# Optimization experiments

Hardware: AMD Instinct MI355X
Metric: run time of the kernel (lower is better)

## Reference

```python
import jax, jax.numpy as jnp
import numpy as np

N_NODES = 50000
N_EDGES = 800000
IN_F, HID_F, OUT_F = 128, 64, 32
N_GRAPHS = 128


def setup_inputs() -> dict:
    key = jax.random.key(0)
    ks = jax.random.split(key, 8)
    x = jax.random.normal(ks[0], (N_NODES, IN_F), dtype=jnp.float32)
    edge_index = jax.random.randint(ks[1], (2, N_EDGES), 0, N_NODES, dtype=jnp.int64)
    edge_features = jax.random.uniform(ks[2], (N_EDGES,), dtype=jnp.float32)
    batch = jnp.sort(jax.random.randint(ks[3], (N_NODES,), 0, N_GRAPHS, dtype=jnp.int64))
    W = jax.random.normal(ks[4], (IN_F, HID_F), dtype=jnp.float32) / np.sqrt(IN_F)
    b = jax.random.normal(ks[5], (HID_F,), dtype=jnp.float32) * 0.01
    W1 = jax.random.normal(ks[6], (HID_F, OUT_F), dtype=jnp.float32) / np.sqrt(HID_F)
    b1 = jax.random.normal(ks[7], (OUT_F,), dtype=jnp.float32) * 0.01
    return {"x": x, "edge_index": edge_index, "edge_features": edge_features,
            "batch": batch, "num_graphs": N_GRAPHS, "W": W, "b": b, "W1": W1, "b1": b1}


def _gcn_conv(x, edge_index, edge_weight, W, b):
    # Standard GCNConv: add self-loops (weight 1), symmetric normalization,
    # transform-then-aggregate.
    n = x.shape[0]
    loop = jnp.arange(n, dtype=edge_index.dtype)
    src = jnp.concatenate([edge_index[0], loop])
    dst = jnp.concatenate([edge_index[1], loop])
    ew = jnp.concatenate([edge_weight, jnp.ones((n,), edge_weight.dtype)])
    deg = jax.ops.segment_sum(ew, dst, num_segments=n)          # [N]
    dinv = jnp.where(deg > 0, jax.lax.rsqrt(deg), 0.0)
    norm = dinv[src] * ew * dinv[dst]                           # [E+N]
    h = x @ W                                                   # [N, H]
    msg = h[src] * norm[:, None]                                # gather + scale
    out = jax.ops.segment_sum(msg, dst, num_segments=n)         # scatter-add
    return out + b


def reference(x, edge_index, edge_features, batch, num_graphs, W, b, W1, b1):
    h = _gcn_conv(x, edge_index, edge_features, W, b)
    h = jnp.tanh(h)
    # dropout is identity at inference
    node_embeddings = h
    sums = jax.ops.segment_sum(h, batch, num_segments=num_graphs)           # [G, H]
    cnts = jax.ops.segment_sum(jnp.ones((h.shape[0],), h.dtype), batch,
                               num_segments=num_graphs)                      # [G]
    graph_embeddings = sums / jnp.maximum(cnts, 1.0)[:, None]
    graph_embeddings = jnp.tanh(graph_embeddings @ W1 + b1)
    return (graph_embeddings, node_embeddings)
```

## Files before the change

### kernel.cpp

```cpp
#include <hip/hip_runtime.h>
#include <hip/hip_fp16.h>
#include <math.h>

#define N_NODES  50000
#define N_EDGES  800000
#define IN_F     128
#define HID_F    64
#define OUT_F    32
#define N_GRAPHS 128
#define SCAN_BLOCKS  ((N_NODES + 255) / 256)
#define GEMM_BLOCKS  ((N_NODES + 127) / 128)
#define HISTO_BLOCKS ((N_EDGES + 255) / 256)

__global__ __launch_bounds__(256) void fused_gemm_histo(const float* __restrict__ x,
                                                        const float* __restrict__ W,
                                                        __half* __restrict__ hs_h,
                                                        const int* __restrict__ dst,
                                                        int* __restrict__ cnt,
                                                        int* __restrict__ epos) {
    __shared__ float Ws[IN_F][HID_F];
    if (blockIdx.x >= GEMM_BLOCKS) {
        int e = (blockIdx.x - GEMM_BLOCKS) * 256 + threadIdx.x;
        if (e < N_EDGES) epos[e] = atomicAdd(&cnt[dst[e]], 1);
        return;
    }

    int tid = threadIdx.x;
    for (int i = tid * 4; i < IN_F * HID_F; i += 256 * 4) {
        *(float4*)&((float*)Ws)[i] = *(const float4*)&W[i];
    }
    __syncthreads();

    int r0 = blockIdx.x * 128 + (tid >> 2);
    int r1 = r0 + 64;
    int c0 = (tid & 3) * 16;
    if (r0 >= N_NODES) return;
    bool has1 = (r1 < N_NODES);

    float acc0[16], acc1[16];
#pragma unroll
    for (int j = 0; j < 16; ++j) { acc0[j] = 0.0f; acc1[j] = 0.0f; }

    const float* xr0 = x + (size_t)r0 * IN_F;
    const float* xr1 = x + (size_t)r1 * IN_F;
    for (int k = 0; k < IN_F; k += 4) {
        float4 xa = *(const float4*)&xr0[k];
        float4 xb = has1 ? *(const float4*)&xr1[k] : make_float4(0, 0, 0, 0);
#pragma unroll
        for (int j = 0; j < 16; ++j) {
            float w0 = Ws[k + 0][c0 + j];
            float w1 = Ws[k + 1][c0 + j];
            float w2 = Ws[k + 2][c0 + j];
            float w3 = Ws[k + 3][c0 + j];
            acc0[j] += xa.x * w0 + xa.y * w1 + xa.z * w2 + xa.w * w3;
            acc1[j] += xb.x * w0 + xb.y * w1 + xb.z * w2 + xb.w * w3;
        }
    }
    __half* hr0 = hs_h + (size_t)r0 * HID_F + c0;
#pragma unroll
    for (int j = 0; j < 16; j += 2) {
        *(__half2*)&hr0[j] = __floats2half2_rn(acc0[j], acc0[j + 1]);
    }
    if (has1) {
        __half* hr1 = hs_h + (size_t)r1 * HID_F + c0;
#pragma unroll
        for (int j = 0; j < 16; j += 2) {
            *(__half2*)&hr1[j] = __floats2half2_rn(acc1[j], acc1[j + 1]);
        }
    }
}

__global__ __launch_bounds__(256) void scan_partial_kernel(const int* __restrict__ cnt,
                                                           int* __restrict__ partials) {
    __shared__ int red[4];
    int i = blockIdx.x * 256 + threadIdx.x;
    int v = (i < N_NODES) ? cnt[i] : 0;
#pragma unroll
    for (int off = 32; off; off >>= 1) v += __shfl_down(v, off, 64);
    int w = threadIdx.x >> 6;
    if ((threadIdx.x & 63) == 0) red[w] = v;
    __syncthreads();
    if (threadIdx.x == 0) partials[blockIdx.x] = red[0] + red[1] + red[2] + red[3];
}

__global__ __launch_bounds__(256) void scan_top_kernel(const int* __restrict__ partials,
                                                       int* __restrict__ ppref) {
    __shared__ int buf[256];
    int t = threadIdx.x;
    buf[t] = (t < SCAN_BLOCKS) ? partials[t] : 0;
    __syncthreads();
    for (int off = 1; off < 256; off <<= 1) {
        int v = (t >= off) ? buf[t - off] : 0;
        __syncthreads();
        buf[t] += v;
        __syncthreads();
    }
    if (t < SCAN_BLOCKS) ppref[t] = (t > 0) ? buf[t - 1] : 0;
}

__global__ __launch_bounds__(256) void scan_final_kernel(const int* __restrict__ cnt,
                                                         const int* __restrict__ ppref,
                                                         int* __restrict__ offsets) {
    __shared__ int buf[256];
    int t = threadIdx.x;
    int i = blockIdx.x * 256 + t;
    int v = (i < N_NODES) ? cnt[i] : 0;
    buf[t] = v;
    __syncthreads();
    for (int off = 1; off < 256; off <<= 1) {
        int x = (t >= off) ? buf[t - off] : 0;
        __syncthreads();
        buf[t] += x;
        __syncthreads();
    }
    if (i < N_NODES) offsets[i] = ppref[blockIdx.x] + buf[t] - v;
}

__global__ __launch_bounds__(256) void bucket_kernel(const int* __restrict__ src,
                                                     const int* __restrict__ dst,
                                                     const float* __restrict__ ew,
                                                     const int* __restrict__ epos,
                                                     const int* __restrict__ offsets,
                                                     int2* __restrict__ edat) {
    int e = blockIdx.x * 256 + threadIdx.x;
    if (e < N_EDGES) {
        int d   = dst[e];
        int pos = offsets[d] + epos[e];
        edat[pos] = make_int2(src[e], __float_as_int(ew[e]));
    }
}

__global__ __launch_bounds__(256) void degw_kernel(const int* __restrict__ offsets,
                                                   const int* __restrict__ cnt,
                                                   const int2* __restrict__ edat,
                                                   float* __restrict__ dinv) {
    int n = blockIdx.x * 256 + threadIdx.x;
    if (n >= N_NODES) return;
    int beg = offsets[n], end = beg + cnt[n];
    float s = 1.0f;
    for (int j = beg; j < end; ++j) s += __int_as_float(edat[j].y);
    dinv[n] = 1.0f / sqrtf(s);
}

__global__ __launch_bounds__(256) void aggregate_kernel(const __half* __restrict__ hs_h,
                                                        const int* __restrict__ offsets,
                                                        const int* __restrict__ cnt,
                                                        const int2* __restrict__ edat,
                                                        const float* __restrict__ dinv,
                                                        const float* __restrict__ b,
                                                        float* __restrict__ nout) {
    int node = blockIdx.x * 4 + (threadIdx.x >> 6);
    if (node >= N_NODES) return;
    int lane = threadIdx.x & 63;
    int half = lane >> 5;
    int fl   = lane & 31;
    int beg  = offsets[node];
    int end  = beg + cnt[node];

    float ax0 = 0.0f, ay0 = 0.0f, ax1 = 0.0f, ay1 = 0.0f;
    int j = beg + half;
    for (; j + 2 < end; j += 4) {
        int2 e0 = edat[j];
        int2 e1 = edat[j + 2];
        float w0 = dinv[e0.x] * __int_as_float(e0.y);
        float w1 = dinv[e1.x] * __int_as_float(e1.y);
        float2 h0 = __half22float2(*(const __half2*)&hs_h[(size_t)e0.x * HID_F + 2 * fl]);
        float2 h1 = __half22float2(*(const __half2*)&hs_h[(size_t)e1.x * HID_F + 2 * fl]);
        ax0 += h0.x * w0; ay0 += h0.y * w0;
        ax1 += h1.x * w1; ay1 += h1.y * w1;
    }
    if (j < end) {
        int2 e0 = edat[j];
        float w0 = dinv[e0.x] * __int_as_float(e0.y);
        float2 h0 = __half22float2(*(const __half2*)&hs_h[(size_t)e0.x * HID_F + 2 * fl]);
        ax0 += h0.x * w0; ay0 += h0.y * w0;
    }

    float sx = ax0 + ax1;
    float sy = ay0 + ay1;
    sx += __shfl_xor(sx, 32, 64);
    sy += __shfl_xor(sy, 32, 64);

    if (half == 0) {
        float dn = dinv[node];
        float2 hself = __half22float2(*(const __half2*)&hs_h[(size_t)node * HID_F + 2 * fl]);
        float2 bb = *(const float2*)&b[2 * fl];
        float vx = dn * (sx + hself.x * dn) + bb.x;
        float vy = dn * (sy + hself.y * dn) + bb.y;
        *(float2*)&nout[(size_t)node * HID_F + 2 * fl] = make_float2(tanhf(vx), tanhf(vy));
    }
}

__global__ void bounds_kernel(const int* __restrict__ batch, int* __restrict__ bounds) {
    int g = threadIdx.x;
    if (g > N_GRAPHS) return;
    int lo = 0, hi = N_NODES;
    while (lo < hi) {
        int m = (lo + hi) >> 1;
        if (batch[m] < g) lo = m + 1; else hi = m;
    }
    bounds[g] = lo;
}

__global__ __launch_bounds__(256) void pool_kernel(const float* __restrict__ ne,
                                                   const int* __restrict__ bounds,
                                                   const float* __restrict__ W1,
                                                   const float* __restrict__ b1,
                                                   float* __restrict__ gout) {
    __shared__ float part[4][HID_F];
    __shared__ float mean_s[HID_F];
    int g  = blockIdx.x;
    int f  = threadIdx.x & 63;
    int w  = threadIdx.x >> 6;
    int lo = bounds[g], hi = bounds[g + 1];

    float s = 0.0f;
    for (int i = lo + w; i < hi; i += 4) s += ne[(size_t)i * HID_F + f];
    part[w][f] = s;
    __syncthreads();

    if (w == 0) {
        float m   = part[0][f] + part[1][f] + part[2][f] + part[3][f];
        float cnt = (float)(hi - lo);
        mean_s[f] = m / fmaxf(cnt, 1.0f);
    }
    __syncthreads();

    int o = threadIdx.x;
    if (o < OUT_F) {
        float acc = b1[o];
        for (int k = 0; k < HID_F; ++k) acc += mean_s[k] * W1[k * OUT_F + o];
        gout[(size_t)g * OUT_F + o] = tanhf(acc);
    }
}

extern "C" void kernel_launch(void* const* d_in, const int* in_sizes, int n_in,
                              void* d_out, int out_size, void* d_ws, size_t ws_size,
                              hipStream_t stream) {
    const float* x   = (const float*)d_in[0];
    const int*   ei  = (const int*)d_in[1];
    const float* ew  = (const float*)d_in[2];
    const int*   bat = (const int*)d_in[3];
    const float* W   = (const float*)d_in[5];
    const float* b   = (const float*)d_in[6];
    const float* W1  = (const float*)d_in[7];
    const float* b1  = (const float*)d_in[8];

    const int* src = ei;
    const int* dst = ei + N_EDGES;

    float* gout = (float*)d_out;
    float* nout = (float*)d_out + (size_t)N_GRAPHS * OUT_F;

    float*  ws_f     = (float*)d_ws;
    float*  dinv     = ws_f;
    __half* hs_h     = (__half*)(ws_f + 50000);
    int*    cnt      = (int*)(ws_f + 1650000);
    int*    offsets  = (int*)(ws_f + 1700000);
    int*    partials = (int*)(ws_f + 1750000);
    int*    ppref    = (int*)(ws_f + 1750256);
    int*    epos     = (int*)(ws_f + 1750512);
    int2*   edat     = (int2*)(ws_f + 2550512);
    int*    bounds   = (int*)(ws_f + 4150512);

    hipMemsetAsync(cnt, 0, (size_t)N_NODES * sizeof(int), stream);

    fused_gemm_histo<<<GEMM_BLOCKS + HISTO_BLOCKS, 256, 0, stream>>>(
        x, W, hs_h, dst, cnt, epos);

    scan_partial_kernel<<<SCAN_BLOCKS, 256, 0, stream>>>(cnt, partials);
    scan_top_kernel<<<1, 256, 0, stream>>>(partials, ppref);
    scan_final_kernel<<<SCAN_BLOCKS, 256, 0, stream>>>(cnt, ppref, offsets);

    bucket_kernel<<<HISTO_BLOCKS, 256, 0, stream>>>(src, dst, ew, epos,
                                                    offsets, edat);

    degw_kernel<<<SCAN_BLOCKS, 256, 0, stream>>>(offsets, cnt, edat, dinv);

    aggregate_kernel<<<(N_NODES + 3) / 4, 256, 0, stream>>>(hs_h, offsets, cnt, edat,
                                                            dinv, b, nout);

    bounds_kernel<<<1, 256, 0, stream>>>(bat, bounds);
    pool_kernel<<<N_GRAPHS, 256, 0, stream>>>(nout, bounds, W1, b1, gout);
}
```

Baseline: 232.0 us.

## Interleave edge histogram atomics into GEMM blocks and fold bounds search into pool

```diff
diff --git a/kernel.cpp b/kernel.cpp
--- a/kernel.cpp
+++ b/kernel.cpp
@@ -11,6 +11,7 @@
 #define SCAN_BLOCKS  ((N_NODES + 255) / 256)
 #define GEMM_BLOCKS  ((N_NODES + 127) / 128)
 #define HISTO_BLOCKS ((N_EDGES + 255) / 256)
+#define EPT 8
 
 __global__ __launch_bounds__(256) void fused_gemm_histo(const float* __restrict__ x,
                                                         const float* __restrict__ W,
@@ -19,13 +20,16 @@
                                                         int* __restrict__ cnt,
                                                         int* __restrict__ epos) {
     __shared__ float Ws[IN_F][HID_F];
-    if (blockIdx.x >= GEMM_BLOCKS) {
-        int e = (blockIdx.x - GEMM_BLOCKS) * 256 + threadIdx.x;
-        if (e < N_EDGES) epos[e] = atomicAdd(&cnt[dst[e]], 1);
-        return;
-    }
-
-    int tid = threadIdx.x;
+    int tid   = threadIdx.x;
+    int ebase = blockIdx.x * (256 * EPT) + tid;
+
+    int epv[EPT];
+#pragma unroll
+    for (int i = 0; i < EPT; ++i) {
+        int e = ebase + i * 256;
+        if (e < N_EDGES) epv[i] = atomicAdd(&cnt[dst[e]], 1);
+    }
+
     for (int i = tid * 4; i < IN_F * HID_F; i += 256 * 4) {
         *(float4*)&((float*)Ws)[i] = *(const float4*)&W[i];
     }
@@ -34,39 +38,46 @@
     int r0 = blockIdx.x * 128 + (tid >> 2);
     int r1 = r0 + 64;
     int c0 = (tid & 3) * 16;
-    if (r0 >= N_NODES) return;
-    bool has1 = (r1 < N_NODES);
-
-    float acc0[16], acc1[16];
-#pragma unroll
-    for (int j = 0; j < 16; ++j) { acc0[j] = 0.0f; acc1[j] = 0.0f; }
-
-    const float* xr0 = x + (size_t)r0 * IN_F;
-    const float* xr1 = x + (size_t)r1 * IN_F;
-    for (int k = 0; k < IN_F; k += 4) {
-        float4 xa = *(const float4*)&xr0[k];
-        float4 xb = has1 ? *(const float4*)&xr1[k] : make_float4(0, 0, 0, 0);
-#pragma unroll
-        for (int j = 0; j < 16; ++j) {
-            float w0 = Ws[k + 0][c0 + j];
-            float w1 = Ws[k + 1][c0 + j];
-            float w2 = Ws[k + 2][c0 + j];
-            float w3 = Ws[k + 3][c0 + j];
-            acc0[j] += xa.x * w0 + xa.y * w1 + xa.z * w2 + xa.w * w3;
-            acc1[j] += xb.x * w0 + xb.y * w1 + xb.z * w2 + xb.w * w3;
-        }
-    }
-    __half* hr0 = hs_h + (size_t)r0 * HID_F + c0;
-#pragma unroll
-    for (int j = 0; j < 16; j += 2) {
-        *(__half2*)&hr0[j] = __floats2half2_rn(acc0[j], acc0[j + 1]);
-    }
-    if (has1) {
-        __half* hr1 = hs_h + (size_t)r1 * HID_F + c0;
+    if (r0 < N_NODES) {
+        bool has1 = (r1 < N_NODES);
+
+        float acc0[16], acc1[16];
+#pragma unroll
+        for (int j = 0; j < 16; ++j) { acc0[j] = 0.0f; acc1[j] = 0.0f; }
+
+        const float* xr0 = x + (size_t)r0 * IN_F;
+        const float* xr1 = x + (size_t)r1 * IN_F;
+        for (int k = 0; k < IN_F; k += 4) {
+            float4 xa = *(const float4*)&xr0[k];
+            float4 xb = has1 ? *(const float4*)&xr1[k] : make_float4(0, 0, 0, 0);
+#pragma unroll
+            for (int j = 0; j < 16; ++j) {
+                float w0 = Ws[k + 0][c0 + j];
+                float w1 = Ws[k + 1][c0 + j];
+                float w2 = Ws[k + 2][c0 + j];
+                float w3 = Ws[k + 3][c0 + j];
+                acc0[j] += xa.x * w0 + xa.y * w1 + xa.z * w2 + xa.w * w3;
+                acc1[j] += xb.x * w0 + xb.y * w1 + xb.z * w2 + xb.w * w3;
+            }
+        }
+        __half* hr0 = hs_h + (size_t)r0 * HID_F + c0;
 #pragma unroll
         for (int j = 0; j < 16; j += 2) {
-            *(__half2*)&hr1[j] = __floats2half2_rn(acc1[j], acc1[j + 1]);
-        }
+            *(__half2*)&hr0[j] = __floats2half2_rn(acc0[j], acc0[j + 1]);
+        }
+        if (has1) {
+            __half* hr1 = hs_h + (size_t)r1 * HID_F + c0;
+#pragma unroll
+            for (int j = 0; j < 16; j += 2) {
+                *(__half2*)&hr1[j] = __floats2half2_rn(acc1[j], acc1[j + 1]);
+            }
+        }
+    }
+
+#pragma unroll
+    for (int i = 0; i < EPT; ++i) {
+        int e = ebase + i * 256;
+        if (e < N_EDGES) epos[e] = epv[i];
     }
 }
 
@@ -191,28 +202,30 @@
     }
 }
 
-__global__ void bounds_kernel(const int* __restrict__ batch, int* __restrict__ bounds) {
-    int g = threadIdx.x;
-    if (g > N_GRAPHS) return;
-    int lo = 0, hi = N_NODES;
-    while (lo < hi) {
-        int m = (lo + hi) >> 1;
-        if (batch[m] < g) lo = m + 1; else hi = m;
-    }
-    bounds[g] = lo;
-}
-
 __global__ __launch_bounds__(256) void pool_kernel(const float* __restrict__ ne,
-                                                   const int* __restrict__ bounds,
+                                                   const int* __restrict__ batch,
                                                    const float* __restrict__ W1,
                                                    const float* __restrict__ b1,
                                                    float* __restrict__ gout) {
     __shared__ float part[4][HID_F];
     __shared__ float mean_s[HID_F];
-    int g  = blockIdx.x;
-    int f  = threadIdx.x & 63;
-    int w  = threadIdx.x >> 6;
-    int lo = bounds[g], hi = bounds[g + 1];
+    __shared__ int   range_s[2];
+    int g = blockIdx.x;
+
+    if (threadIdx.x < 2) {
+        int target = g + threadIdx.x;
+        int lo = 0, hi = N_NODES;
+        while (lo < hi) {
+            int m = (lo + hi) >> 1;
+            if (batch[m] < target) lo = m + 1; else hi = m;
+        }
+        range_s[threadIdx.x] = lo;
+    }
+    __syncthreads();
+    int lo = range_s[0], hi = range_s[1];
+
+    int f = threadIdx.x & 63;
+    int w = threadIdx.x >> 6;
 
     float s = 0.0f;
     for (int i = lo + w; i < hi; i += 4) s += ne[(size_t)i * HID_F + f];
@@ -261,12 +274,10 @@
     int*    ppref    = (int*)(ws_f + 1750256);
     int*    epos     = (int*)(ws_f + 1750512);
     int2*   edat     = (int2*)(ws_f + 2550512);
-    int*    bounds   = (int*)(ws_f + 4150512);
 
     hipMemsetAsync(cnt, 0, (size_t)N_NODES * sizeof(int), stream);
 
-    fused_gemm_histo<<<GEMM_BLOCKS + HISTO_BLOCKS, 256, 0, stream>>>(
-        x, W, hs_h, dst, cnt, epos);
+    fused_gemm_histo<<<GEMM_BLOCKS, 256, 0, stream>>>(x, W, hs_h, dst, cnt, epos);
 
     scan_partial_kernel<<<SCAN_BLOCKS, 256, 0, stream>>>(cnt, partials);
     scan_top_kernel<<<1, 256, 0, stream>>>(partials, ppref);
@@ -280,6 +291,5 @@
     aggregate_kernel<<<(N_NODES + 3) / 4, 256, 0, stream>>>(hs_h, offsets, cnt, edat,
                                                             dinv, b, nout);
 
-    bounds_kernel<<<1, 256, 0, stream>>>(bat, bounds);
-    pool_kernel<<<N_GRAPHS, 256, 0, stream>>>(nout, bounds, W1, b1, gout);
-}
+    pool_kernel<<<N_GRAPHS, 256, 0, stream>>>(nout, bat, W1, b1, gout);
+}
```

Result: no change. 236.0 us (+1.7%).
